# Kernel optimization log

Measured on AMD Instinct MI355X. Metric: run time of the kernel, lower is better.

The kernel has to match this reference:

```python
import jax, jax.numpy as jnp
import numpy as np

D_MODEL = 768
N_HEADS = 24
D_HEAD = 64
D_STATE = 64
CHUNK = 64
D_INNER = N_HEADS * D_HEAD  # 1536
N_LAYER = 24
B_SZ = 2
SEQ = 8192
RMS_EPS = 1.1920929e-07  # torch.finfo(float32).eps (nn.RMSNorm default eps)


def setup_inputs() -> dict:
    key = jax.random.key(0)
    ks = jax.random.split(key, 8)
    proj = N_HEADS * (1 + 2 * D_STATE)
    return {
        "hidden_states": jax.random.normal(ks[0], (B_SZ, SEQ, D_MODEL), jnp.float32),
        "norm_w": jnp.ones((D_MODEL,), jnp.float32),
        "in_proj_w": jax.random.normal(ks[1], (2 * D_INNER, D_MODEL), jnp.float32) * 0.02,
        "in_proj_b": jnp.zeros((2 * D_INNER,), jnp.float32),
        "conv_w": jax.random.normal(ks[2], (D_INNER, 1, 4), jnp.float32) * 0.25,
        "conv_b": jnp.zeros((D_INNER,), jnp.float32),
        "x_proj_w": jax.random.normal(ks[3], (proj, D_INNER), jnp.float32) * 0.02,
        "x_proj_b": jnp.zeros((proj,), jnp.float32),
        "A_log": jnp.full((N_HEADS,), float(np.log(0.5)), jnp.float32),
        "log2_alpha_base": jnp.full((N_HEADS,), -0.15, jnp.float32),
        "log2_beta": jnp.zeros((N_HEADS,), jnp.float32),
        "surprise_ema": jnp.ones((N_HEADS,), jnp.float32),
        "out_proj_w": jax.random.normal(ks[4], (D_MODEL, D_INNER), jnp.float32) * 0.02,
        "out_proj_b": jnp.zeros((D_MODEL,), jnp.float32),
        "res_gate": jnp.full((1,), 1.0 / float(np.sqrt(2 * N_LAYER)), jnp.float32),
    }


def _block_forward(hidden_states, norm_w, in_proj_w, in_proj_b, conv_w, conv_b,
                   x_proj_w, x_proj_b, A_log, log2_alpha_base, log2_beta,
                   surprise_ema, out_proj_w, out_proj_b, res_gate):
    residual = hidden_states
    b, L, _ = hidden_states.shape

    # RMSNorm
    x = hidden_states * jax.lax.rsqrt(
        jnp.mean(hidden_states ** 2, axis=-1, keepdims=True) + RMS_EPS) * norm_w

    # in_proj, split x/z
    xz = hidden_states_proj = x @ in_proj_w.T + in_proj_b
    x, z = jnp.split(xz, 2, axis=-1)  # [b, L, d_inner] each

    # causal depthwise conv1d (kernel 4, padding 3, then truncate to L)
    xc = jnp.transpose(x, (0, 2, 1))  # [b, C, L]
    xc = jax.lax.conv_general_dilated(
        xc, conv_w, window_strides=(1,), padding=[(3, 3)],
        dimension_numbers=("NCH", "OIH", "NCH"), feature_group_count=D_INNER)
    xc = xc[:, :, :L] + conv_b[None, :, None]
    x = jax.nn.silu(jnp.transpose(xc, (0, 2, 1)))  # [b, L, d_inner]

    # x_proj -> dt, B, C
    xp = (x @ x_proj_w.T + x_proj_b).reshape(b, L, N_HEADS, 1 + 2 * D_STATE)
    dt = xp[..., 0]
    B_ssm = xp[..., 1:1 + D_STATE]
    C_ssm = xp[..., 1 + D_STATE:]
    B_ssm = B_ssm / jnp.maximum(jnp.linalg.norm(B_ssm, axis=-1, keepdims=True), 1e-12)
    C_ssm = C_ssm / jnp.maximum(jnp.linalg.norm(C_ssm, axis=-1, keepdims=True), 1e-12)

    A = jnp.clip(A_log, -2.3, -0.01)[None, None, :]  # [1,1,H]
    dt_scale = jnp.clip(jax.nn.softplus(jnp.clip(dt, -10.0, 10.0)), 0.01, 10.0)
    A = jnp.clip(A * dt_scale, -20.0, -0.001)  # [b, L, H]

    X = x.reshape(b, L, N_HEADS, D_HEAD)

    # ---- chunked surprise-gated SSD (L divisible by CHUNK) ----
    n = L // CHUNK
    X_t = X.reshape(b, n, CHUNK, N_HEADS, D_HEAD).transpose(0, 3, 1, 2, 4)      # b h n c d
    A_t = A.reshape(b, n, CHUNK, N_HEADS).transpose(0, 3, 1, 2)                 # b h n c
    B_t = B_ssm.reshape(b, n, CHUNK, N_HEADS, D_STATE).transpose(0, 3, 1, 2, 4) # b h n c s
    C_t = C_ssm.reshape(b, n, CHUNK, N_HEADS, D_STATE).transpose(0, 3, 1, 2, 4) # b h n c s

    BX = jnp.einsum("bhncs,bhncd->bhnsd", B_t, X_t)
    chunk_surprise = jnp.mean(BX ** 2, axis=(-1, -2))  # [b, h, n]

    # surprise gate (training=True: EMA updated first, no_grad)
    mean_s = jax.lax.stop_gradient(jnp.mean(chunk_surprise, axis=(0, 2)))
    ema = 0.99 * surprise_ema + 0.01 * mean_s
    normalized = chunk_surprise / (ema[None, :, None] + 1e-6)
    alpha_base = 1.0 - 2.0 ** jnp.clip(log2_alpha_base, -3.32, -0.015)  # [H]
    beta = 2.0 ** jnp.clip(log2_beta, -2.0, 2.0)                        # [H]
    boost_pos = jax.nn.relu(jnp.tanh(beta[None, :, None] * normalized))
    ab = alpha_base[None, :, None]
    alpha = jnp.clip(ab + (1.0 - ab) * boost_pos, 0.01, 0.999)          # [b, h, n]

    A_mod = A_t * (1.0 - alpha)[..., None]          # b h n c
    A_cs = jnp.cumsum(A_mod, axis=-1)               # b h n c

    # intra-chunk: L[i,j] = exp(cs_i - cs_j) for i >= j
    diff = A_cs[..., :, None] - A_cs[..., None, :]  # b h n c c
    mask = jnp.tril(jnp.ones((CHUNK, CHUNK), bool))
    Lmat = jnp.where(mask, jnp.exp(diff), 0.0)
    CB = jnp.einsum("bhnid,bhnjd->bhnij", C_t, B_t)
    Y_intra = jnp.einsum("bhnij,bhnjd->bhnid", Lmat * CB, X_t)

    # inter-chunk recurrence
    decay_chunk = jnp.exp(jnp.sum(A_mod, axis=-1))              # b h n
    decay_to_end = jnp.exp(A_cs[..., -1:] - A_cs)               # b h n c
    h_chunk_final = jnp.einsum("bhnc,bhncs,bhncd->bhnsd",
                               decay_to_end, B_t, X_t)           # b h n s d

    def step(carry, inp):
        d, hf = inp  # d: [b,h], hf: [b,h,s,d]
        new = d[..., None, None] * carry + hf
        return new, carry  # emit state BEFORE this chunk

    carry0 = jnp.zeros((b, N_HEADS, D_STATE, D_HEAD), X.dtype)
    _, h_inter = jax.lax.scan(
        step, carry0,
        (decay_chunk.transpose(2, 0, 1), h_chunk_final.transpose(2, 0, 1, 3, 4)))
    h_inter = h_inter.transpose(1, 2, 0, 3, 4)  # b h n s d

    decay_from_start = jnp.exp(A_cs)  # b h n c
    Y_inter = jnp.einsum("bhnis,bhnsp,bhni->bhnip", C_t, h_inter, decay_from_start)

    Y = (Y_intra + Y_inter).transpose(0, 2, 3, 1, 4).reshape(b, L, D_INNER)

    # gate + out proj + gated residual
    y = jnp.clip(Y, -100.0, 100.0) * jax.nn.sigmoid(z)
    out = jnp.clip(y @ out_proj_w.T + out_proj_b, -100.0, 100.0)
    return residual + out * res_gate


def reference(hidden_states, norm_w, in_proj_w, in_proj_b, conv_w, conv_b,
              x_proj_w, x_proj_b, A_log, log2_alpha_base, log2_beta,
              surprise_ema, out_proj_w, out_proj_b, res_gate):
    return _block_forward(hidden_states, norm_w, in_proj_w, in_proj_b, conv_w,
                          conv_b, x_proj_w, x_proj_b, A_log, log2_alpha_base,
                          log2_beta, surprise_ema, out_proj_w, out_proj_b, res_gate)
```

## Files before the change

### kernel.cpp

```cpp
#include <hip/hip_runtime.h>
#include <hip/hip_bf16.h>
#include <cstdint>
#include <cstddef>

#define L_SEQ   8192
#define DMODEL  768
#define NHEADS  24
#define DINNER  1536
#define NPROJ   3096
#define NPROJP  3200
#define XPS     3072
#define NTOK    16384
#define BT      8192
#define RMS_EPS 1.1920929e-07f

typedef __hip_bfloat16 bf16;
typedef __attribute__((ext_vector_type(8))) short bf8v;
typedef __attribute__((ext_vector_type(4))) float f4v;

__device__ __forceinline__ float clampf(float x, float lo, float hi) {
    return fminf(fmaxf(x, lo), hi);
}
__device__ __forceinline__ float bf2f(bf16 v) { return __bfloat162float(v); }
__device__ __forceinline__ bf16  f2bf(float v) { return __float2bfloat16(v); }
__device__ __forceinline__ short f2bs(float v) {
    bf16 b = __float2bfloat16(v);
    return *reinterpret_cast<short*>(&b);
}
__device__ __forceinline__ float bs2f(short v) {
    return __uint_as_float(((unsigned)(unsigned short)v) << 16);
}
__device__ __forceinline__ void st1(float* p, float v) { *p = v; }
__device__ __forceinline__ void st1(bf16* p, float v) { *p = f2bf(v); }
__device__ __forceinline__ void st4(bf16* p, float4 v) {
    p[0] = f2bf(v.x); p[1] = f2bf(v.y); p[2] = f2bf(v.z); p[3] = f2bf(v.w);
}

#define GLOAD16(gsrc, ldst) __builtin_amdgcn_global_load_lds( \
    (const __attribute__((address_space(1))) void*)(gsrc),    \
    (__attribute__((address_space(3))) void*)(ldst), 16, 0, 0)

__global__ __launch_bounds__(256) void k_cvt(const float* __restrict__ s,
                                             bf16* __restrict__ d, int n4) {
    int i = blockIdx.x * 256 + threadIdx.x;
    if (i < n4) {
        float4 v = *(const float4*)&s[i * 4];
        st4(&d[i * 4], v);
    }
}
__global__ __launch_bounds__(256) void k_zero(bf16* __restrict__ d, int n) {
    int i = blockIdx.x * 256 + threadIdx.x;
    if (i < n) d[i] = f2bf(0.f);
}
__global__ __launch_bounds__(256) void k_wdt(const float* __restrict__ w2,
                                             const float* __restrict__ b2,
                                             bf16* __restrict__ wdt,
                                             float* __restrict__ bdt) {
    int i = blockIdx.x * 256 + threadIdx.x;
    if (i < 128 * DINNER) {
        int h = i / DINNER, c = i - h * DINNER;
        wdt[i] = f2bf(h < 24 ? w2[(size_t)(h * 129) * DINNER + c] : 0.f);
    }
    if (i < 128) bdt[i] = (i < 24) ? b2[i * 129] : 0.f;
}

__global__ __launch_bounds__(256) void k_rmsnorm(const float* __restrict__ hs,
                                                 const float* __restrict__ w,
                                                 bf16* __restrict__ xn) {
    int t = blockIdx.x;
    const float* p = hs + (size_t)t * DMODEL;
    float s = 0.f;
    for (int i = threadIdx.x; i < DMODEL; i += 256) { float v = p[i]; s += v * v; }
    for (int off = 32; off; off >>= 1) s += __shfl_xor(s, off, 64);
    __shared__ float ws4[4];
    int lane = threadIdx.x & 63, wv = threadIdx.x >> 6;
    if (lane == 0) ws4[wv] = s;
    __syncthreads();
    s = ws4[0] + ws4[1] + ws4[2] + ws4[3];
    float r = 1.0f / sqrtf(s * (1.0f / DMODEL) + RMS_EPS);
    bf16* o = xn + (size_t)t * DMODEL;
    for (int i = threadIdx.x; i < DMODEL; i += 256) o[i] = f2bf(p[i] * r * w[i]);
}

template <typename TC, int EPI>
__global__ __launch_bounds__(256) void k_mgemm(const bf16* __restrict__ A,
                                               const bf16* __restrict__ B,
                                               const float* __restrict__ bias,
                                               TC* __restrict__ C,
                                               int M, int N, int K,
                                               const float* __restrict__ resid,
                                               const float* __restrict__ gatep) {
    __shared__ short As[2][128 * 32];
    __shared__ short Bs[2][128 * 32];
    int tid = threadIdx.x;
    int lane = tid & 63, w = tid >> 6;

    int gx = gridDim.x, gy = gridDim.y;
    int bid = blockIdx.y * gx + blockIdx.x;
    int xcd = bid & 7, idx = bid >> 3;
    int bys = gy >> 3;
    int gby = bys < 8 ? bys : 8;
    int sg  = idx / (gx * gby);
    int rem = idx - sg * (gx * gby);
    int bx  = rem / gby;
    int byl = rem - bx * gby;
    int by  = xcd * bys + sg * gby + byl;
    int m0 = by * 128, n0 = bx * 128;

    int wm = (w >> 1) << 6, wn = (w & 1) << 6;

    const size_t rowskip = (size_t)16 * K * 2;
    const char* Ag = (const char*)(A + (size_t)(m0 + (w << 5) + (lane >> 2)) * K) + (lane & 3) * 16;
    const char* Bg = (const char*)(B + (size_t)(n0 + (w << 5) + (lane >> 2)) * K) + (lane & 3) * 16;
    short* Al0 = &As[0][(w << 5) * 32];
    short* Bl0 = &Bs[0][(w << 5) * 32];
    short* Al1 = &As[1][(w << 5) * 32];
    short* Bl1 = &Bs[1][(w << 5) * 32];

    f4v acc[4][4];
#pragma unroll
    for (int i = 0; i < 4; ++i)
#pragma unroll
        for (int j = 0; j < 4; ++j) acc[i][j] = (f4v){0.f, 0.f, 0.f, 0.f};

    auto stage = [&](int buf, int k0) {
        size_t kb = (size_t)k0 * 2;
        short* Al = buf ? Al1 : Al0;
        short* Bl = buf ? Bl1 : Bl0;
        GLOAD16(Ag + kb,           Al);
        GLOAD16(Ag + kb + rowskip, Al + 16 * 32);
        GLOAD16(Bg + kb,           Bl);
        GLOAD16(Bg + kb + rowskip, Bl + 16 * 32);
    };

    stage(0, 0);
    int cur = 0;
    int row16 = lane & 15, kg = (lane >> 4) << 3;
    for (int k0 = 0; k0 < K; k0 += 32) {
        __syncthreads();
        if (k0 + 32 < K) stage(cur ^ 1, k0 + 32);
        const short* Ab = As[cur];
        const short* Bb = Bs[cur];
        bf8v af[4], bfv[4];
#pragma unroll
        for (int fm = 0; fm < 4; ++fm)
            af[fm] = *(const bf8v*)&Ab[(wm + (fm << 4) + row16) * 32 + kg];
#pragma unroll
        for (int fn = 0; fn < 4; ++fn)
            bfv[fn] = *(const bf8v*)&Bb[(wn + (fn << 4) + row16) * 32 + kg];
#pragma unroll
        for (int fm = 0; fm < 4; ++fm)
#pragma unroll
            for (int fn = 0; fn < 4; ++fn)
                acc[fm][fn] = __builtin_amdgcn_mfma_f32_16x16x32_bf16(
                    af[fm], bfv[fn], acc[fm][fn], 0, 0, 0);
        cur ^= 1;
    }

    float gate = (EPI == 1) ? *gatep : 0.f;
    int rbase = m0 + wm + ((lane >> 4) << 2);
#pragma unroll
    for (int fn = 0; fn < 4; ++fn) {
        int col = n0 + wn + (fn << 4) + (lane & 15);
        if (col >= N) continue;
        float bc = bias[col];
#pragma unroll
        for (int fm = 0; fm < 4; ++fm) {
#pragma unroll
            for (int r = 0; r < 4; ++r) {
                int row = rbase + (fm << 4) + r;
                float v = acc[fm][fn][r] + bc;
                if (EPI == 1)
                    v = resid[(size_t)row * N + col] + clampf(v, -100.f, 100.f) * gate;
                st1(&C[(size_t)row * N + col], v);
            }
        }
    }
}

template <typename TC, int EPI>
__global__ __launch_bounds__(512) void k_mgemm2(const bf16* __restrict__ A,
                                                const bf16* __restrict__ B,
                                                const float* __restrict__ bias,
                                                TC* __restrict__ C,
                                                int M, int N, int K) {
    __shared__ short AB[2][384 * 32];
    int tid = threadIdx.x;
    int lane = tid & 63, w = tid >> 6;

    int gx = gridDim.x, gy = gridDim.y;
    int bid = blockIdx.y * gx + blockIdx.x;
    int xcd = bid & 7, idx = bid >> 3;
    int bys = gy >> 3;
    int gby = bys < 4 ? bys : 4;
    int sg  = idx / (gx * gby);
    int rem = idx - sg * (gx * gby);
    int bx  = rem / gby;
    int byl = rem - bx * gby;
    int by  = xcd * bys + sg * gby + byl;
    int m0 = by * 256, n0 = bx * 128;

    int wm = (w >> 1) << 6, wn = (w & 1) << 6;

    const bf16* gp[3];
#pragma unroll
    for (int i = 0; i < 3; ++i) {
        int g = i * 512 + tid;
        int row = g >> 2, cq = (g & 3) << 3;
        gp[i] = (row < 256 ? A + (size_t)(m0 + row) * K
                           : B + (size_t)(n0 + row - 256) * K) + cq;
    }

    f4v acc[4][4];
#pragma unroll
    for (int i = 0; i < 4; ++i)
#pragma unroll
        for (int j = 0; j < 4; ++j) acc[i][j] = (f4v){0.f, 0.f, 0.f, 0.f};

    auto stage = [&](int buf, int k0) {
#pragma unroll
        for (int i = 0; i < 3; ++i) {
            short* dst = &AB[buf][(i * 512 + (w << 6)) * 8];
            GLOAD16((const char*)gp[i] + (size_t)k0 * 2, dst);
        }
    };

    stage(0, 0);
    int cur = 0;
    int row16 = lane & 15, kg = (lane >> 4) << 3;
    for (int k0 = 0; k0 < K; k0 += 32) {
        __syncthreads();
        if (k0 + 32 < K) stage(cur ^ 1, k0 + 32);
        const short* Ab = AB[cur];
        const short* Bb = AB[cur] + 256 * 32;
        bf8v af[4], bfv[4];
#pragma unroll
        for (int fm = 0; fm < 4; ++fm)
            af[fm] = *(const bf8v*)&Ab[(wm + (fm << 4) + row16) * 32 + kg];
#pragma unroll
        for (int fn = 0; fn < 4; ++fn)
            bfv[fn] = *(const bf8v*)&Bb[(wn + (fn << 4) + row16) * 32 + kg];
#pragma unroll
        for (int fm = 0; fm < 4; ++fm)
#pragma unroll
            for (int fn = 0; fn < 4; ++fn)
                acc[fm][fn] = __builtin_amdgcn_mfma_f32_16x16x32_bf16(
                    af[fm], bfv[fn], acc[fm][fn], 0, 0, 0);
        cur ^= 1;
    }

    int rbase = m0 + wm + ((lane >> 4) << 2);
#pragma unroll
    for (int fn = 0; fn < 4; ++fn) {
        int col = n0 + wn + (fn << 4) + (lane & 15);
        if (col >= N) continue;
        float bc = bias[col];
        int dst = col;
        if (EPI == 2) {
            int hh = col / 129, q = col - hh * 129;
            if (q == 0) continue;
            dst = hh * 128 + q - 1;
        }
#pragma unroll
        for (int fm = 0; fm < 4; ++fm) {
#pragma unroll
            for (int r = 0; r < 4; ++r) {
                int row = rbase + (fm << 4) + r;
                float v = acc[fm][fn][r] + bc;
                if (EPI == 2) st1(&C[(size_t)row * XPS + dst], v);
                else          st1(&C[(size_t)row * N + col], v);
            }
        }
    }
}

__global__ __launch_bounds__(192) void k_conv4(const bf16* __restrict__ x,
                                               const float* __restrict__ cw,
                                               const float* __restrict__ cb,
                                               bf16* __restrict__ xc) {
    int c0 = threadIdx.x * 8;
    int r0 = blockIdx.x * 4;
    bf8v xr[7];
    const bf8v z8 = (bf8v){0, 0, 0, 0, 0, 0, 0, 0};
#pragma unroll
    for (int j = 0; j < 7; ++j) {
        int rr = r0 - 3 + j;
        xr[j] = (rr >= 0) ? *(const bf8v*)(const void*)(x + (size_t)rr * DINNER + c0) : z8;
    }
    float wk[4][8], cbv[8];
#pragma unroll
    for (int j = 0; j < 8; ++j) {
        cbv[j] = cb[c0 + j];
#pragma unroll
        for (int k = 0; k < 4; ++k) wk[k][j] = cw[(c0 + j) * 4 + k];
    }
#pragma unroll
    for (int i = 0; i < 4; ++i) {
        bf8v o;
#pragma unroll
        for (int j = 0; j < 8; ++j) {
            float a = cbv[j];
#pragma unroll
            for (int k = 0; k < 4; ++k) a += wk[k][j] * bs2f(xr[i + k][j]);
            o[j] = f2bs(a / (1.f + expf(-a)));
        }
        *(bf8v*)(xc + (size_t)(r0 + i) * DINNER + c0) = o;
    }
}

__global__ __launch_bounds__(256) void k_prep(const bf16* __restrict__ xp,
                                              const bf16* __restrict__ dtb,
                                              const float* __restrict__ A_log,
                                              float* __restrict__ Aarr,
                                              float* __restrict__ invB,
                                              float* __restrict__ invC) {
    int wv = threadIdx.x >> 6, lane = threadIdx.x & 63;
    int idx = blockIdx.x * 4 + wv;
    int t = idx / 24, h = idx - t * 24;
    const bf16* base = xp + (size_t)t * XPS + h * 128;
    float b = bf2f(base[lane]), c = bf2f(base[64 + lane]);
    float sb = b * b, sc = c * c;
    for (int off = 32; off; off >>= 1) {
        sb += __shfl_xor(sb, off, 64);
        sc += __shfl_xor(sc, off, 64);
    }
    if (lane == 0) {
        invB[idx] = 1.f / fmaxf(sqrtf(sb), 1e-12f);
        invC[idx] = 1.f / fmaxf(sqrtf(sc), 1e-12f);
        float dt = clampf(bf2f(dtb[idx]), -10.f, 10.f);
        float dts = clampf(log1pf(expf(dt)), 0.01f, 10.f);
        float A = clampf(A_log[h], -2.3f, -0.01f) * dts;
        Aarr[idx] = clampf(A, -20.f, -0.001f);
    }
}

__global__ __launch_bounds__(256) void k_surprise_all(const bf16* __restrict__ xp,
                                                      const bf16* __restrict__ xc,
                                                      const float* __restrict__ invB,
                                                      float* __restrict__ cs) {
    int g = blockIdx.x;
    int cg = g / 24, h = g - cg * 24;
    int b = cg >> 7, nl = cg & 127;
    int t0 = cg * 64;
    size_t cs_idx = (size_t)(b * 24 + h) * 128 + nl;
    __shared__ short Ws[64 * 72];
    __shared__ short Xt[64 * 72];
    int tid = threadIdx.x;
#pragma unroll
    for (int half = 0; half < 2; ++half) {
        int tau = tid + half * 256;
        int c = tau >> 3, s0 = (tau & 7) << 3;
        int t = t0 + c;
        float ib = invB[t * 24 + h];
        bf8v Bv = *(const bf8v*)(const void*)(xp + (size_t)t * XPS + h * 128 + s0);
        bf8v Xv = *(const bf8v*)(const void*)(xc + (size_t)t * DINNER + h * 64 + s0);
#pragma unroll
        for (int u = 0; u < 8; ++u) {
            Ws[(s0 + u) * 72 + c] = f2bs(bs2f(Bv[u]) * ib);
            Xt[(s0 + u) * 72 + c] = Xv[u];
        }
    }
    __syncthreads();
    int w = tid >> 6, lane = tid & 63;
    int r16 = lane & 15, kq = (lane >> 4) << 3;
    int strip = w << 4;
    f4v acc[4];
#pragma unroll
    for (int dt = 0; dt < 4; ++dt) acc[dt] = (f4v){0.f, 0.f, 0.f, 0.f};
#pragma unroll
    for (int ks = 0; ks < 2; ++ks) {
        bf8v af = *(const bf8v*)&Ws[(strip + r16) * 72 + ks * 32 + kq];
#pragma unroll
        for (int dt = 0; dt < 4; ++dt) {
            bf8v bf_ = *(const bf8v*)&Xt[((dt << 4) + r16) * 72 + ks * 32 + kq];
            acc[dt] = __builtin_amdgcn_mfma_f32_16x16x32_bf16(af, bf_, acc[dt], 0, 0, 0);
        }
    }
    float ss = 0.f;
#pragma unroll
    for (int dt = 0; dt < 4; ++dt)
#pragma unroll
        for (int r = 0; r < 4; ++r) ss += acc[dt][r] * acc[dt][r];
    for (int off = 32; off; off >>= 1) ss += __shfl_xor(ss, off, 64);
    __shared__ float ws4[4];
    if (lane == 0) ws4[w] = ss;
    __syncthreads();
    if (tid == 0) cs[cs_idx] = (ws4[0] + ws4[1] + ws4[2] + ws4[3]) * (1.f / 4096.f);
}

__global__ __launch_bounds__(256) void k_alpha(const float* __restrict__ cs,
                                               const float* __restrict__ ema0,
                                               const float* __restrict__ l2ab,
                                               const float* __restrict__ l2b,
                                               float* __restrict__ alpha) {
    int h = blockIdx.x, tid = threadIdx.x;
    int b = tid >> 7, n = tid & 127;
    int gi = (b * 24 + h) * 128 + n;
    float v = cs[gi];
    float s = v;
    for (int off = 32; off; off >>= 1) s += __shfl_xor(s, off, 64);
    __shared__ float ws4[4];
    int lane = tid & 63, wv = tid >> 6;
    if (lane == 0) ws4[wv] = s;
    __syncthreads();
    float total = ws4[0] + ws4[1] + ws4[2] + ws4[3];
    float ema = 0.99f * ema0[h] + 0.01f * (total * (1.f / 256.f));
    float ab = 1.f - exp2f(clampf(l2ab[h], -3.32f, -0.015f));
    float beta = exp2f(clampf(l2b[h], -2.f, 2.f));
    float nz = v / (ema + 1e-6f);
    float boost = fmaxf(tanhf(beta * nz), 0.f);
    alpha[gi] = clampf(ab + (1.f - ab) * boost, 0.01f, 0.999f);
}

__global__ __launch_bounds__(256) void k_chunk(const bf16* __restrict__ xp,
                                               const bf16* __restrict__ xc,
                                               const float* __restrict__ invB,
                                               const float* __restrict__ invC,
                                               const float* __restrict__ Aarr,
                                               const float* __restrict__ alpha,
                                               bf16* __restrict__ ybuf,
                                               bf16* __restrict__ hf,
                                               float* __restrict__ dchunk,
                                               int b) {
    int g = blockIdx.x;
    int h = g >> 7, nl = g & 127;
    int t0 = nl * 64;
    size_t gidx = (size_t)(b * 24 + h) * 128 + nl;
    size_t hbase = (size_t)g * 4096;
    float alp = alpha[gidx];
    __shared__ short Cs[64 * 72];
    __shared__ short Bs[64 * 72];
    __shared__ short Ws[64 * 72];
    __shared__ short Xt[64 * 72];
    __shared__ float Acs[64];
    __shared__ float dte[64];
    int tid = threadIdx.x;
    if (tid < 64) {
        float a = Aarr[(size_t)(t0 + tid) * 24 + h] * (1.f - alp);
        for (int off = 1; off < 64; off <<= 1) {
            float u = __shfl_up(a, off, 64);
            if (tid >= off) a += u;
        }
        Acs[tid] = a;
        float total = __shfl(a, 63, 64);
        dte[tid] = expf(total - a);
        if (tid == 0) dchunk[gidx] = expf(total);
    }
    __syncthreads();
#pragma unroll
    for (int half = 0; half < 2; ++half) {
        int tau = tid + half * 256;
        int c = tau >> 3, s0 = (tau & 7) << 3;
        int t = t0 + c;
        const bf16* bp = xp + (size_t)t * XPS + h * 128;
        float ib = invB[t * 24 + h], ic2 = invC[t * 24 + h];
        float dc = dte[c];
        bf8v Bv = *(const bf8v*)(const void*)(bp + s0);
        bf8v Cv = *(const bf8v*)(const void*)(bp + 64 + s0);
        bf8v Xv = *(const bf8v*)(const void*)(xc + (size_t)t * DINNER + h * 64 + s0);
        bf8v Bsc, Csc;
#pragma unroll
        for (int u = 0; u < 8; ++u) {
            float bv = bs2f(Bv[u]) * ib;
            Bsc[u] = f2bs(bv);
            Csc[u] = f2bs(bs2f(Cv[u]) * ic2);
            Ws[(s0 + u) * 72 + c] = f2bs(bv * dc);
            Xt[(s0 + u) * 72 + c] = Xv[u];
        }
        *(bf8v*)&Bs[c * 72 + s0] = Bsc;
        *(bf8v*)&Cs[c * 72 + s0] = Csc;
    }
    __syncthreads();
    int w = tid >> 6, lane = tid & 63;
    int r16 = lane & 15, kq = (lane >> 4) << 3;
    int strip = w << 4;
    f4v acb[4], ach[4];
#pragma unroll
    for (int jt = 0; jt < 4; ++jt) {
        acb[jt] = (f4v){0.f, 0.f, 0.f, 0.f};
        ach[jt] = (f4v){0.f, 0.f, 0.f, 0.f};
    }
#pragma unroll
    for (int ks = 0; ks < 2; ++ks) {
        bf8v afc = *(const bf8v*)&Cs[(strip + r16) * 72 + ks * 32 + kq];
        bf8v afw = *(const bf8v*)&Ws[(strip + r16) * 72 + ks * 32 + kq];
#pragma unroll
        for (int jt = 0; jt < 4; ++jt) {
            bf8v bb = *(const bf8v*)&Bs[((jt << 4) + r16) * 72 + ks * 32 + kq];
            acb[jt] = __builtin_amdgcn_mfma_f32_16x16x32_bf16(afc, bb, acb[jt], 0, 0, 0);
            bf8v xx = *(const bf8v*)&Xt[((jt << 4) + r16) * 72 + ks * 32 + kq];
            ach[jt] = __builtin_amdgcn_mfma_f32_16x16x32_bf16(afw, xx, ach[jt], 0, 0, 0);
        }
    }
    int rbase = strip + ((lane >> 4) << 2);
#pragma unroll
    for (int dt = 0; dt < 4; ++dt) {
        int d = (dt << 4) + r16;
#pragma unroll
        for (int r = 0; r < 4; ++r)
            hf[hbase + (size_t)(rbase + r) * 64 + d] = f2bf(ach[dt][r]);
    }
    __syncthreads();
    short* Ms = Cs;
#pragma unroll
    for (int jt = 0; jt < 4; ++jt) {
        int j = (jt << 4) + r16;
        float aj = Acs[j];
#pragma unroll
        for (int r = 0; r < 4; ++r) {
            int i = rbase + r;
            float m = (j <= i) ? expf(Acs[i] - aj) * acb[jt][r] : 0.f;
            Ms[i * 72 + j] = f2bs(m);
        }
    }
    __syncthreads();
    f4v acy[4];
#pragma unroll
    for (int dt = 0; dt < 4; ++dt) acy[dt] = (f4v){0.f, 0.f, 0.f, 0.f};
#pragma unroll
    for (int ks = 0; ks < 2; ++ks) {
        bf8v afm = *(const bf8v*)&Ms[(strip + r16) * 72 + ks * 32 + kq];
#pragma unroll
        for (int dt = 0; dt < 4; ++dt) {
            bf8v xx = *(const bf8v*)&Xt[((dt << 4) + r16) * 72 + ks * 32 + kq];
            acy[dt] = __builtin_amdgcn_mfma_f32_16x16x32_bf16(afm, xx, acy[dt], 0, 0, 0);
        }
    }
#pragma unroll
    for (int dt = 0; dt < 4; ++dt) {
        int d = (dt << 4) + r16;
#pragma unroll
        for (int r = 0; r < 4; ++r) {
            int i = rbase + r;
            ybuf[(size_t)(t0 + i) * DINNER + h * 64 + d] = f2bf(acy[dt][r]);
        }
    }
}

__global__ __launch_bounds__(256) void k_scan(bf16* __restrict__ hf,
                                              const float* __restrict__ dchunk,
                                              int b) {
    int h = blockIdx.x >> 4;
    int e = ((blockIdx.x & 15) << 8) + threadIdx.x;
    size_t abase = (size_t)h * 128 * 4096 + e;
    const float* dcp = dchunk + (size_t)(b * 24 + h) * 128;
    float c = 0.f;
    float v0 = bf2f(hf[abase]);
    float v1 = bf2f(hf[abase + 1 * 4096]);
    float v2 = bf2f(hf[abase + 2 * 4096]);
    float v3 = bf2f(hf[abase + 3 * 4096]);
    for (int nl = 0; nl < 128; nl += 4) {
        float p0 = (nl + 4 < 128) ? bf2f(hf[abase + (size_t)(nl + 4) * 4096]) : 0.f;
        float p1 = (nl + 5 < 128) ? bf2f(hf[abase + (size_t)(nl + 5) * 4096]) : 0.f;
        float p2 = (nl + 6 < 128) ? bf2f(hf[abase + (size_t)(nl + 6) * 4096]) : 0.f;
        float p3 = (nl + 7 < 128) ? bf2f(hf[abase + (size_t)(nl + 7) * 4096]) : 0.f;
        hf[abase + (size_t)nl * 4096] = f2bf(c);
        c = dcp[nl] * c + v0;
        hf[abase + (size_t)(nl + 1) * 4096] = f2bf(c);
        c = dcp[nl + 1] * c + v1;
        hf[abase + (size_t)(nl + 2) * 4096] = f2bf(c);
        c = dcp[nl + 2] * c + v2;
        hf[abase + (size_t)(nl + 3) * 4096] = f2bf(c);
        c = dcp[nl + 3] * c + v3;
        v0 = p0; v1 = p1; v2 = p2; v3 = p3;
    }
}

__global__ __launch_bounds__(256) void k_inter(const bf16* __restrict__ xp,
                                               const float* __restrict__ invC,
                                               const float* __restrict__ Aarr,
                                               const float* __restrict__ alpha,
                                               const bf16* __restrict__ hf,
                                               const bf16* __restrict__ zbuf,
                                               bf16* __restrict__ ybuf,
                                               int b) {
    int g = blockIdx.x;
    int h = g >> 7, nl = g & 127;
    int t0 = nl * 64;
    size_t gidx = (size_t)(b * 24 + h) * 128 + nl;
    size_t hbase = (size_t)g * 4096;
    float alp = alpha[gidx];
    __shared__ short Cs[64 * 72];
    __shared__ short Ht[64 * 72];
    __shared__ float dfs[64];
    int tid = threadIdx.x;
    if (tid < 64) {
        float a = Aarr[(size_t)(t0 + tid) * 24 + h] * (1.f - alp);
        for (int off = 1; off < 64; off <<= 1) {
            float u = __shfl_up(a, off, 64);
            if (tid >= off) a += u;
        }
        dfs[tid] = expf(a);
    }
#pragma unroll
    for (int half = 0; half < 2; ++half) {
        int tau = tid + half * 256;
        int c = tau >> 3, s0 = (tau & 7) << 3;
        int t = t0 + c;
        float ic2 = invC[t * 24 + h];
        bf8v Cv = *(const bf8v*)(const void*)(xp + (size_t)t * XPS + h * 128 + 64 + s0);
        bf8v Hv = *(const bf8v*)(const void*)(hf + hbase + (size_t)c * 64 + s0);
        bf8v Csc;
#pragma unroll
        for (int u = 0; u < 8; ++u) {
            Csc[u] = f2bs(bs2f(Cv[u]) * ic2);
            Ht[(s0 + u) * 72 + c] = Hv[u];
        }
        *(bf8v*)&Cs[c * 72 + s0] = Csc;
    }
    __syncthreads();
    int w = tid >> 6, lane = tid & 63;
    int r16 = lane & 15, kq = (lane >> 4) << 3;
    int strip = w << 4;
    f4v acc[4];
#pragma unroll
    for (int dt = 0; dt < 4; ++dt) acc[dt] = (f4v){0.f, 0.f, 0.f, 0.f};
#pragma unroll
    for (int ks = 0; ks < 2; ++ks) {
        bf8v af = *(const bf8v*)&Cs[(strip + r16) * 72 + ks * 32 + kq];
#pragma unroll
        for (int dt = 0; dt < 4; ++dt) {
            bf8v hfr = *(const bf8v*)&Ht[((dt << 4) + r16) * 72 + ks * 32 + kq];
            acc[dt] = __builtin_amdgcn_mfma_f32_16x16x32_bf16(af, hfr, acc[dt], 0, 0, 0);
        }
    }
    int ibase = strip + ((lane >> 4) << 2);
#pragma unroll
    for (int dt = 0; dt < 4; ++dt) {
        int d = (dt << 4) + r16;
#pragma unroll
        for (int r = 0; r < 4; ++r) {
            int i = ibase + r;
            float df = dfs[i];
            size_t yoff = (size_t)(t0 + i) * DINNER + h * 64 + d;
            float Y = clampf(bf2f(ybuf[yoff]) + df * acc[dt][r], -100.f, 100.f);
            float zz = bf2f(zbuf[yoff]);
            ybuf[yoff] = f2bf(Y / (1.f + expf(-zz)));
        }
    }
}

extern "C" void kernel_launch(void* const* d_in, const int* in_sizes, int n_in,
                              void* d_out, int out_size, void* d_ws, size_t ws_size,
                              hipStream_t stream) {
    const float* hs     = (const float*)d_in[0];
    const float* norm_w = (const float*)d_in[1];
    const float* w1     = (const float*)d_in[2];
    const float* b1     = (const float*)d_in[3];
    const float* cw     = (const float*)d_in[4];
    const float* cbias  = (const float*)d_in[5];
    const float* w2     = (const float*)d_in[6];
    const float* b2     = (const float*)d_in[7];
    const float* A_log  = (const float*)d_in[8];
    const float* l2ab   = (const float*)d_in[9];
    const float* l2b    = (const float*)d_in[10];
    const float* ema0   = (const float*)d_in[11];
    const float* w3     = (const float*)d_in[12];
    const float* b3     = (const float*)d_in[13];
    const float* rg     = (const float*)d_in[14];
    float* out = (float*)d_out;

    char* base = (char*)d_ws;
    size_t off = 0;
    auto alloc = [&](size_t bytes) -> void* {
        void* p = base + off;
        off += (bytes + 255) & ~(size_t)255;
        return p;
    };
    bf16* w1bf  = (bf16*)alloc((size_t)2 * DINNER * DMODEL * 2);
    bf16* w2bf  = (bf16*)alloc((size_t)NPROJP * DINNER * 2);
    bf16* w3bf  = (bf16*)alloc((size_t)DMODEL * DINNER * 2);
    bf16* wdt   = (bf16*)alloc((size_t)128 * DINNER * 2);
    float* bdt  = (float*)alloc((size_t)128 * 4);
    bf16* xnb   = (bf16*)alloc((size_t)BT * DMODEL * 2);
    bf16* ybuf  = (bf16*)alloc((size_t)BT * DINNER * 2);
    bf16* hf    = (bf16*)alloc((size_t)NHEADS * 128 * 4096 * 2);
    bf16* dtb   = (bf16*)alloc((size_t)NTOK * 24 * 2);
    float* cs   = (float*)alloc((size_t)6144 * 4);
    float* alp  = (float*)alloc((size_t)6144 * 4);
    float* dch  = (float*)alloc((size_t)6144 * 4);
    bf16* xp    = (bf16*)alloc((size_t)NTOK * XPS * 2);
    float* Aarr = (float*)alloc((size_t)NTOK * 24 * 4);
    float* invB = (float*)alloc((size_t)NTOK * 24 * 4);
    float* invC = (float*)alloc((size_t)NTOK * 24 * 4);
    bf16* xbuf  = ybuf;
    bf16* xc_all = (bf16*)d_out;

    {
        int n1 = 2 * DINNER * DMODEL / 4, n2 = NPROJ * DINNER / 4, n3 = DMODEL * DINNER / 4;
        k_cvt<<<(n1 + 255) / 256, 256, 0, stream>>>(w1, w1bf, n1);
        k_cvt<<<(n2 + 255) / 256, 256, 0, stream>>>(w2, w2bf, n2);
        k_cvt<<<(n3 + 255) / 256, 256, 0, stream>>>(w3, w3bf, n3);
        int nz = (NPROJP - NPROJ) * DINNER;
        k_zero<<<(nz + 255) / 256, 256, 0, stream>>>(w2bf + (size_t)NPROJ * DINNER, nz);
        k_wdt<<<(128 * DINNER + 255) / 256, 256, 0, stream>>>(w2, b2, wdt, bdt);
    }

    const dim3 gXb(DINNER / 128, BT / 256);
    const dim3 gOb(DMODEL / 128, BT / 128);
    const dim3 gPall(NPROJP / 128, NTOK / 256);
    const dim3 gDt(1, NTOK / 128);

    for (int bt = 0; bt < 2; ++bt) {
        size_t t0 = (size_t)bt * BT;
        k_rmsnorm<<<BT, 256, 0, stream>>>(hs + t0 * DMODEL, norm_w, xnb);
        k_mgemm2<bf16, 0><<<gXb, 512, 0, stream>>>(xnb, w1bf, b1, xbuf,
                                                   BT, DINNER, DMODEL);
        k_conv4<<<BT / 4, 192, 0, stream>>>(xbuf, cw, cbias, xc_all + t0 * DINNER);
    }
    k_mgemm2<bf16, 2><<<gPall, 512, 0, stream>>>(xc_all, w2bf, b2, xp,
                                                 NTOK, NPROJ, DINNER);
    k_mgemm<bf16, 0><<<gDt, 256, 0, stream>>>(xc_all, wdt, bdt, dtb,
                                              NTOK, 24, DINNER, nullptr, nullptr);
    k_prep<<<NTOK * 24 / 4, 256, 0, stream>>>(xp, dtb, A_log, Aarr, invB, invC);
    k_surprise_all<<<6144, 256, 0, stream>>>(xp, xc_all, invB, cs);
    k_alpha<<<24, 256, 0, stream>>>(cs, ema0, l2ab, l2b, alp);

    for (int pass = 0; pass < 2; ++pass) {
        int bt = 1 - pass;
        size_t t0 = (size_t)bt * BT;
        bf16* xc = xc_all + t0 * DINNER;
        bf16* zseg = xc;
        const bf16* xpS = xp + t0 * XPS;
        const float* AarrS = Aarr + t0 * 24;
        const float* invBS = invB + t0 * 24;
        const float* invCS = invC + t0 * 24;
        k_chunk<<<NHEADS * 128, 256, 0, stream>>>(xpS, xc, invBS, invCS, AarrS, alp,
                                                  ybuf, hf, dch, bt);
        if (bt == 0)
            k_rmsnorm<<<BT, 256, 0, stream>>>(hs + t0 * DMODEL, norm_w, xnb);
        k_mgemm2<bf16, 0><<<gXb, 512, 0, stream>>>(xnb, w1bf + (size_t)DINNER * DMODEL,
                                                   b1 + DINNER, zseg,
                                                   BT, DINNER, DMODEL);
        k_scan<<<384, 256, 0, stream>>>(hf, dch, bt);
        k_inter<<<NHEADS * 128, 256, 0, stream>>>(xpS, invCS, AarrS, alp, hf, zseg, ybuf, bt);
        k_mgemm<float, 1><<<gOb, 256, 0, stream>>>(ybuf, w3bf, b3, out + t0 * DMODEL,
                                                   BT, DMODEL, DINNER,
                                                   hs + t0 * DMODEL, rg);
    }
}
```

Measured before the change: 778.1 us.

## Fuse x and z in_proj GEMMs and stash z in workspace when space allows

When the workspace is large enough, the first GEMM computes both the x and z halves of in_proj in one launch. The z half is written to a new workspace buffer, so the later per-pass z GEMM and the second RMSNorm recompute are dropped and the pass order becomes natural. This trades 50 MB of extra workspace traffic for fewer launches and no redundant RMSNorm. Whether the fused path runs depends on the workspace size the harness provides.

```diff
diff --git a/kernel.cpp b/kernel.cpp
--- a/kernel.cpp
+++ b/kernel.cpp
@@ -183,7 +183,8 @@
                                                 const bf16* __restrict__ B,
                                                 const float* __restrict__ bias,
                                                 TC* __restrict__ C,
-                                                int M, int N, int K) {
+                                                int M, int N, int K,
+                                                TC* __restrict__ C2) {
     __shared__ short AB[2][384 * 32];
     int tid = threadIdx.x;
     int lane = tid & 63, w = tid >> 6;
@@ -256,10 +257,13 @@
         if (col >= N) continue;
         float bc = bias[col];
         int dst = col;
+        TC* Cp = C;
         if (EPI == 2) {
             int hh = col / 129, q = col - hh * 129;
             if (q == 0) continue;
             dst = hh * 128 + q - 1;
+        } else if (EPI == 3) {
+            if (col >= DINNER) { Cp = C2; dst = col - DINNER; }
         }
 #pragma unroll
         for (int fm = 0; fm < 4; ++fm) {
@@ -267,8 +271,9 @@
             for (int r = 0; r < 4; ++r) {
                 int row = rbase + (fm << 4) + r;
                 float v = acc[fm][fn][r] + bc;
-                if (EPI == 2) st1(&C[(size_t)row * XPS + dst], v);
-                else          st1(&C[(size_t)row * N + col], v);
+                if (EPI == 2)       st1(&C[(size_t)row * XPS + dst], v);
+                else if (EPI == 3)  st1(&Cp[(size_t)row * DINNER + dst], v);
+                else                st1(&C[(size_t)row * N + col], v);
             }
         }
     }
@@ -660,6 +665,8 @@
     const float* rg     = (const float*)d_in[14];
     float* out = (float*)d_out;
 
+    const bool FUSE = ws_size >= (size_t)238000000;
+
     char* base = (char*)d_ws;
     size_t off = 0;
     auto alloc = [&](size_t bytes) -> void* {
@@ -683,6 +690,7 @@
     float* Aarr = (float*)alloc((size_t)NTOK * 24 * 4);
     float* invB = (float*)alloc((size_t)NTOK * 24 * 4);
     float* invC = (float*)alloc((size_t)NTOK * 24 * 4);
+    bf16* zst   = FUSE ? (bf16*)alloc((size_t)NTOK * DINNER * 2) : nullptr;
     bf16* xbuf  = ybuf;
     bf16* xc_all = (bf16*)d_out;
 
@@ -697,6 +705,7 @@
     }
 
     const dim3 gXb(DINNER / 128, BT / 256);
+    const dim3 gXZ(2 * DINNER / 128, BT / 256);
     const dim3 gOb(DMODEL / 128, BT / 128);
     const dim3 gPall(NPROJP / 128, NTOK / 256);
     const dim3 gDt(1, NTOK / 128);
@@ -704,38 +713,63 @@
     for (int bt = 0; bt < 2; ++bt) {
         size_t t0 = (size_t)bt * BT;
         k_rmsnorm<<<BT, 256, 0, stream>>>(hs + t0 * DMODEL, norm_w, xnb);
-        k_mgemm2<bf16, 0><<<gXb, 512, 0, stream>>>(xnb, w1bf, b1, xbuf,
-                                                   BT, DINNER, DMODEL);
+        if (FUSE) {
+            k_mgemm2<bf16, 3><<<gXZ, 512, 0, stream>>>(xnb, w1bf, b1, xbuf,
+                                                       BT, 2 * DINNER, DMODEL,
+                                                       zst + t0 * DINNER);
+        } else {
+            k_mgemm2<bf16, 0><<<gXb, 512, 0, stream>>>(xnb, w1bf, b1, xbuf,
+                                                       BT, DINNER, DMODEL, nullptr);
+        }
         k_conv4<<<BT / 4, 192, 0, stream>>>(xbuf, cw, cbias, xc_all + t0 * DINNER);
     }
     k_mgemm2<bf16, 2><<<gPall, 512, 0, stream>>>(xc_all, w2bf, b2, xp,
-                                                 NTOK, NPROJ, DINNER);
+                                                 NTOK, NPROJ, DINNER, nullptr);
     k_mgemm<bf16, 0><<<gDt, 256, 0, stream>>>(xc_all, wdt, bdt, dtb,
                                               NTOK, 24, DINNER, nullptr, nullptr);
     k_prep<<<NTOK * 24 / 4, 256, 0, stream>>>(xp, dtb, A_log, Aarr, invB, invC);
     k_surprise_all<<<6144, 256, 0, stream>>>(xp, xc_all, invB, cs);
     k_alpha<<<24, 256, 0, stream>>>(cs, ema0, l2ab, l2b, alp);
 
-    for (int pass = 0; pass < 2; ++pass) {
-        int bt = 1 - pass;
-        size_t t0 = (size_t)bt * BT;
-        bf16* xc = xc_all + t0 * DINNER;
-        bf16* zseg = xc;
-        const bf16* xpS = xp + t0 * XPS;
-        const float* AarrS = Aarr + t0 * 24;
-        const float* invBS = invB + t0 * 24;
-        const float* invCS = invC + t0 * 24;
-        k_chunk<<<NHEADS * 128, 256, 0, stream>>>(xpS, xc, invBS, invCS, AarrS, alp,
-                                                  ybuf, hf, dch, bt);
-        if (bt == 0)
-            k_rmsnorm<<<BT, 256, 0, stream>>>(hs + t0 * DMODEL, norm_w, xnb);
-        k_mgemm2<bf16, 0><<<gXb, 512, 0, stream>>>(xnb, w1bf + (size_t)DINNER * DMODEL,
-                                                   b1 + DINNER, zseg,
-                                                   BT, DINNER, DMODEL);
-        k_scan<<<384, 256, 0, stream>>>(hf, dch, bt);
-        k_inter<<<NHEADS * 128, 256, 0, stream>>>(xpS, invCS, AarrS, alp, hf, zseg, ybuf, bt);
-        k_mgemm<float, 1><<<gOb, 256, 0, stream>>>(ybuf, w3bf, b3, out + t0 * DMODEL,
-                                                   BT, DMODEL, DINNER,
-                                                   hs + t0 * DMODEL, rg);
-    }
-}
+    if (FUSE) {
+        for (int bt = 0; bt < 2; ++bt) {
+            size_t t0 = (size_t)bt * BT;
+            bf16* xc = xc_all + t0 * DINNER;
+            const bf16* xpS = xp + t0 * XPS;
+            const float* AarrS = Aarr + t0 * 24;
+            const float* invBS = invB + t0 * 24;
+            const float* invCS = invC + t0 * 24;
+            k_chunk<<<NHEADS * 128, 256, 0, stream>>>(xpS, xc, invBS, invCS, AarrS, alp,
+                                                      ybuf, hf, dch, bt);
+            k_scan<<<384, 256, 0, stream>>>(hf, dch, bt);
+            k_inter<<<NHEADS * 128, 256, 0, stream>>>(xpS, invCS, AarrS, alp, hf,
+                                                      zst + t0 * DINNER, ybuf, bt);
+            k_mgemm<float, 1><<<gOb, 256, 0, stream>>>(ybuf, w3bf, b3, out + t0 * DMODEL,
+                                                       BT, DMODEL, DINNER,
+                                                       hs + t0 * DMODEL, rg);
+        }
+    } else {
+        for (int pass = 0; pass < 2; ++pass) {
+            int bt = 1 - pass;
+            size_t t0 = (size_t)bt * BT;
+            bf16* xc = xc_all + t0 * DINNER;
+            bf16* zseg = xc;
+            const bf16* xpS = xp + t0 * XPS;
+            const float* AarrS = Aarr + t0 * 24;
+            const float* invBS = invB + t0 * 24;
+            const float* invCS = invC + t0 * 24;
+            k_chunk<<<NHEADS * 128, 256, 0, stream>>>(xpS, xc, invBS, invCS, AarrS, alp,
+                                                      ybuf, hf, dch, bt);
+            if (bt == 0)
+                k_rmsnorm<<<BT, 256, 0, stream>>>(hs + t0 * DMODEL, norm_w, xnb);
+            k_mgemm2<bf16, 0><<<gXb, 512, 0, stream>>>(xnb, w1bf + (size_t)DINNER * DMODEL,
+                                                       b1 + DINNER, zseg,
+                                                       BT, DINNER, DMODEL, nullptr);
+            k_scan<<<384, 256, 0, stream>>>(hf, dch, bt);
+            k_inter<<<NHEADS * 128, 256, 0, stream>>>(xpS, invCS, AarrS, alp, hf, zseg, ybuf, bt);
+            k_mgemm<float, 1><<<gOb, 256, 0, stream>>>(ybuf, w3bf, b3, out + t0 * DMODEL,
+                                                       BT, DMODEL, DINNER,
+                                                       hs + t0 * DMODEL, rg);
+        }
+    }
+}
```

Result: no change. 790.6 us (+1.6%).
